# Kernel tuning notes

Hardware: AMD Instinct MI355X
Metric: run time of the kernel (lower is better)

## Reference

```python
import jax, jax.numpy as jnp
import numpy as np

SEQ_LEN = 2048

def setup_inputs() -> dict:
    key = jax.random.key(0)
    kq, kk, kv = jax.random.split(key, 3)
    B, S, D = 8, SEQ_LEN, 64
    q = jax.random.normal(kq, (B, S, D), dtype=jnp.float32)
    k = jax.random.normal(kk, (B, S, D), dtype=jnp.float32)
    v = jax.random.normal(kv, (B, S, D), dtype=jnp.float32)
    return {"q": q, "k": k, "v": v}

def reference(q, k, v):
    # scores: [B, S, S] = q @ k^T  (note: original applies NO 1/sqrt(d) scaling)
    scores = jnp.einsum('bqd,bkd->bqk', q, k)
    S = scores.shape[-1]
    causal = jnp.tril(jnp.ones((S, S), dtype=bool))  # lower-triangular mask
    scores = jnp.where(causal, scores, -jnp.inf)
    weights = jax.nn.softmax(scores, axis=-1)
    return jnp.einsum('bqk,bkd->bqd', weights, v)
```

## Files before the change

kernel.cpp:

```cpp
#include <hip/hip_runtime.h>


#define BATCH 8
#define SEQ 2048
#define DIM 64
#define NEL (BATCH * SEQ * DIM)

typedef __attribute__((ext_vector_type(8))) short short8;
typedef __attribute__((ext_vector_type(4))) float f32x4;

#define MFMA(a, b, c) __builtin_amdgcn_mfma_f32_16x16x32_bf16(a, b, c, 0, 0, 0)

__device__ __forceinline__ unsigned short f2bf(float x) {
    unsigned u = __float_as_uint(x);
    unsigned r = u + 0x7fffu + ((u >> 16) & 1u);
    return (unsigned short)(r >> 16);
}
__device__ __forceinline__ float bf2f(unsigned short h) {
    return __uint_as_float(((unsigned)h) << 16);
}
__device__ __forceinline__ short8 ld8(const unsigned short* p) {
    return *(const short8*)p;
}

__device__ __forceinline__ float dpp_max16(float x) {
    float o;
    o = __int_as_float(__builtin_amdgcn_update_dpp(0, __float_as_int(x), 0xB1, 0xF, 0xF, true));
    x = fmaxf(x, o);
    o = __int_as_float(__builtin_amdgcn_update_dpp(0, __float_as_int(x), 0x4E, 0xF, 0xF, true));
    x = fmaxf(x, o);
    o = __int_as_float(__builtin_amdgcn_update_dpp(0, __float_as_int(x), 0x141, 0xF, 0xF, true));
    x = fmaxf(x, o);
    o = __int_as_float(__builtin_amdgcn_update_dpp(0, __float_as_int(x), 0x140, 0xF, 0xF, true));
    return fmaxf(x, o);
}
__device__ __forceinline__ float dpp_sum16(float x) {
    float o;
    o = __int_as_float(__builtin_amdgcn_update_dpp(0, __float_as_int(x), 0xB1, 0xF, 0xF, true));
    x += o;
    o = __int_as_float(__builtin_amdgcn_update_dpp(0, __float_as_int(x), 0x4E, 0xF, 0xF, true));
    x += o;
    o = __int_as_float(__builtin_amdgcn_update_dpp(0, __float_as_int(x), 0x141, 0xF, 0xF, true));
    x += o;
    o = __int_as_float(__builtin_amdgcn_update_dpp(0, __float_as_int(x), 0x140, 0xF, 0xF, true));
    return x + o;
}

__global__ __launch_bounds__(256) void prep(
    const float* __restrict__ Q, const float* __restrict__ K,
    const float* __restrict__ V,
    unsigned short* __restrict__ Qh, unsigned short* __restrict__ Ql,
    unsigned short* __restrict__ Kh, unsigned short* __restrict__ Kl,
    unsigned short* __restrict__ Vf)
{
    __shared__ unsigned short sT[64][72];
    const int blk = blockIdx.x;
    const int t = threadIdx.x;

    if (blk < 2048) {
        const int idx = (blk * 256 + t) * 4;
        const float* src; unsigned short *dh, *dl; int off;
        if (idx < NEL) { src = Q; dh = Qh; dl = Ql; off = idx; }
        else           { src = K; dh = Kh; dl = Kl; off = idx - NEL; }
        float4 v = *(const float4*)(src + off);
        ushort4 h, l;
        h.x = f2bf(v.x); l.x = f2bf(v.x - bf2f(h.x));
        h.y = f2bf(v.y); l.y = f2bf(v.y - bf2f(h.y));
        h.z = f2bf(v.z); l.z = f2bf(v.z - bf2f(h.z));
        h.w = f2bf(v.w); l.w = f2bf(v.w - bf2f(h.w));
        *(ushort4*)(dh + off) = h;
        *(ushort4*)(dl + off) = l;
        return;
    }

    const int tile = blk - 2048;
    const int b = tile >> 5;
    const int s0 = (tile & 31) * 64;
    const int srow = t >> 4;
    const int d4   = (t & 15) * 4;
#pragma unroll
    for (int i = 0; i < 4; ++i) {
        const int row = srow + i * 16;
        float4 v = *(const float4*)(V + ((size_t)(b * SEQ + s0 + row)) * DIM + d4);
        sT[d4 + 0][row] = f2bf(v.x);
        sT[d4 + 1][row] = f2bf(v.y);
        sT[d4 + 2][row] = f2bf(v.z);
        sT[d4 + 3][row] = f2bf(v.w);
    }
    __syncthreads();
#pragma unroll
    for (int i = 0; i < 2; ++i) {
        const int fid = t + i * 256;
        const int cc  = fid >> 8;
        const int nt  = (fid >> 6) & 3;
        const int l   = fid & 63;
        const int key = cc * 32 + (l >> 4) * 8;
        const int dim = nt * 16 + (l & 15);
        const int c   = (s0 >> 5) + cc;
        unsigned short* dst =
            Vf + ((((size_t)(b * 64 + c)) * 4 + nt) << 9) + l * 8;
        *(float4*)dst = *(const float4*)&sT[dim][key];
    }
}

__global__ __launch_bounds__(256) void attn_main(
    const unsigned short* __restrict__ Qh, const unsigned short* __restrict__ Ql,
    const unsigned short* __restrict__ Kh, const unsigned short* __restrict__ Kl,
    const unsigned short* __restrict__ Vf, float* __restrict__ O)
{
    __shared__ __align__(16) char scratch[4][4352];
    __shared__ float sMl[4][16][2];

    const int bid  = blockIdx.x;
    const int b    = bid & (BATCH - 1);
    const int pair = bid >> 3;

    const int t    = threadIdx.x;
    const int w    = t >> 6;
    const int lane = t & 63;
    const int quad = lane >> 4;
    const int n16  = lane & 15;
    const int boff = b * SEQ;

    unsigned short* sPw = (unsigned short*)scratch[w];
    float*          sOw = (float*)scratch[w];

    for (int half = 0; half < 2; ++half) {
        const int qt = half ? (127 - pair) : pair;
        const int q0 = qt * 16;
        const int q_max = q0 + 15;

        const unsigned short* qp  = Qh + ((size_t)(boff + q0 + n16)) * DIM + quad * 8;
        const unsigned short* qlp = Ql + ((size_t)(boff + q0 + n16)) * DIM + quad * 8;
        short8 qh0 = ld8(qp),  qh1 = ld8(qp + 32);
        short8 ql0 = ld8(qlp), ql1 = ld8(qlp + 32);

        float m0 = -1e30f, m1 = -1e30f, m2 = -1e30f, m3 = -1e30f;
        float l0 = 0.f, l1 = 0.f, l2 = 0.f, l3 = 0.f;
        f32x4 oacc[4];
#pragma unroll
        for (int i = 0; i < 4; ++i) oacc[i] = (f32x4){0.f, 0.f, 0.f, 0.f};

        for (int kb = w * 128; kb <= q_max; kb += 512) {
            const int rem  = q_max - kb;
            const int nsub = min(8, (rem >> 4) + 1);
            const int nchain = (nsub + 1) >> 1;
            f32x4 sacc[8];

#pragma unroll
            for (int gp = 0; gp < 4; ++gp) {
                const int stA = 2 * gp, stB = stA + 1;
                if (stA < nsub) {
                    const size_t krA = (size_t)(boff + kb + stA * 16 + n16) * DIM + quad * 8;
                    short8 khA0 = ld8(Kh + krA), khA1 = ld8(Kh + krA + 32);
                    short8 klA0 = ld8(Kl + krA), klA1 = ld8(Kl + krA + 32);
                    const bool okB = (stB < nsub);
                    const size_t krB = (size_t)(boff + kb + stB * 16 + n16) * DIM + quad * 8;
                    short8 khB0, khB1, klB0, klB1;
                    if (okB) {
                        khB0 = ld8(Kh + krB); khB1 = ld8(Kh + krB + 32);
                        klB0 = ld8(Kl + krB); klB1 = ld8(Kl + krB + 32);
                    }
                    f32x4 accA = (f32x4){0.f, 0.f, 0.f, 0.f};
                    accA = MFMA(qh0, khA0, accA);
                    accA = MFMA(qh1, khA1, accA);
                    accA = MFMA(qh0, klA0, accA);
                    accA = MFMA(qh1, klA1, accA);
                    accA = MFMA(ql0, khA0, accA);
                    accA = MFMA(ql1, khA1, accA);
                    sacc[stA] = accA;
                    if (okB) {
                        f32x4 accB = (f32x4){0.f, 0.f, 0.f, 0.f};
                        accB = MFMA(qh0, khB0, accB);
                        accB = MFMA(qh1, khB1, accB);
                        accB = MFMA(qh0, klB0, accB);
                        accB = MFMA(qh1, klB1, accB);
                        accB = MFMA(ql0, khB0, accB);
                        accB = MFMA(ql1, khB1, accB);
                        sacc[stB] = accB;
                    } else {
                        sacc[stB] = (f32x4){-1e30f, -1e30f, -1e30f, -1e30f};
                    }
                } else {
                    sacc[stA] = (f32x4){-1e30f, -1e30f, -1e30f, -1e30f};
                    sacc[stB] = (f32x4){-1e30f, -1e30f, -1e30f, -1e30f};
                }
            }

            if (kb + 127 > q0) {
#pragma unroll
                for (int st = 0; st < 8; ++st) {
                    if (st < nsub) {
                        const int key = kb + st * 16 + n16;
#pragma unroll
                        for (int r = 0; r < 4; ++r)
                            if (key > q0 + quad * 4 + r) sacc[st][r] = -1e30f;
                    }
                }
            }

            float mt0 = sacc[0][0], mt1 = sacc[0][1], mt2 = sacc[0][2], mt3 = sacc[0][3];
#pragma unroll
            for (int st = 1; st < 8; ++st) {
                mt0 = fmaxf(mt0, sacc[st][0]);
                mt1 = fmaxf(mt1, sacc[st][1]);
                mt2 = fmaxf(mt2, sacc[st][2]);
                mt3 = fmaxf(mt3, sacc[st][3]);
            }
            mt0 = dpp_max16(mt0); mt1 = dpp_max16(mt1);
            mt2 = dpp_max16(mt2); mt3 = dpp_max16(mt3);
            const float mn0 = fmaxf(m0, mt0), mn1 = fmaxf(m1, mt1);
            const float mn2 = fmaxf(m2, mt2), mn3 = fmaxf(m3, mt3);
            const float a0 = __expf(m0 - mn0), a1 = __expf(m1 - mn1);
            const float a2 = __expf(m2 - mn2), a3 = __expf(m3 - mn3);
            m0 = mn0; m1 = mn1; m2 = mn2; m3 = mn3;

            float ps0 = 0.f, ps1 = 0.f, ps2 = 0.f, ps3 = 0.f;
            const int stmax = 2 * nchain;
#pragma unroll
            for (int st = 0; st < 8; ++st) {
                if (st < stmax) {
                    float p0 = 0.f, p1 = 0.f, p2 = 0.f, p3 = 0.f;
                    if (st < nsub) {
                        p0 = __expf(sacc[st][0] - mn0);
                        p1 = __expf(sacc[st][1] - mn1);
                        p2 = __expf(sacc[st][2] - mn2);
                        p3 = __expf(sacc[st][3] - mn3);
                        ps0 += p0; ps1 += p1; ps2 += p2; ps3 += p3;
                    }
                    const int col = st * 16 + n16;
                    sPw[(quad * 4 + 0) * 136 + col] = f2bf(p0);
                    sPw[(quad * 4 + 1) * 136 + col] = f2bf(p1);
                    sPw[(quad * 4 + 2) * 136 + col] = f2bf(p2);
                    sPw[(quad * 4 + 3) * 136 + col] = f2bf(p3);
                }
            }
            ps0 = dpp_sum16(ps0); ps1 = dpp_sum16(ps1);
            ps2 = dpp_sum16(ps2); ps3 = dpp_sum16(ps3);
            l0 = l0 * a0 + ps0; l1 = l1 * a1 + ps1;
            l2 = l2 * a2 + ps2; l3 = l3 * a3 + ps3;
#pragma unroll
            for (int nt = 0; nt < 4; ++nt) {
                oacc[nt][0] *= a0; oacc[nt][1] *= a1;
                oacc[nt][2] *= a2; oacc[nt][3] *= a3;
            }

#pragma unroll
            for (int ch = 0; ch < 4; ++ch) {
                if (ch < nchain) {
                    short8 pa = ld8(&sPw[n16 * 136 + ch * 32 + quad * 8]);
                    const size_t cbase =
                        (((size_t)(b * 64 + (kb >> 5) + ch)) * 4) << 9;
#pragma unroll
                    for (int nt = 0; nt < 4; ++nt) {
                        short8 vv = ld8(Vf + cbase + (nt << 9) + lane * 8);
                        oacc[nt] = MFMA(pa, vv, oacc[nt]);
                    }
                }
            }
        }

#pragma unroll
        for (int nt = 0; nt < 4; ++nt)
#pragma unroll
            for (int r = 0; r < 4; ++r)
                sOw[(quad * 4 + r) * 68 + nt * 16 + n16] = oacc[nt][r];
        if (n16 == 0) {
            sMl[w][quad * 4 + 0][0] = m0; sMl[w][quad * 4 + 0][1] = l0;
            sMl[w][quad * 4 + 1][0] = m1; sMl[w][quad * 4 + 1][1] = l1;
            sMl[w][quad * 4 + 2][0] = m2; sMl[w][quad * 4 + 2][1] = l2;
            sMl[w][quad * 4 + 3][0] = m3; sMl[w][quad * 4 + 3][1] = l3;
        }
        __syncthreads();

        const int row  = t >> 4;
        const int col4 = (t & 15) * 4;
        float M = fmaxf(fmaxf(sMl[0][row][0], sMl[1][row][0]),
                        fmaxf(sMl[2][row][0], sMl[3][row][0]));
        float L = 0.f;
        float ox = 0.f, oy = 0.f, oz = 0.f, ow = 0.f;
#pragma unroll
        for (int wv = 0; wv < 4; ++wv) {
            const float ew = __expf(sMl[wv][row][0] - M);
            L += ew * sMl[wv][row][1];
            const float* op = (const float*)scratch[wv] + row * 68 + col4;
            ox += ew * op[0]; oy += ew * op[1]; oz += ew * op[2]; ow += ew * op[3];
        }
        const float inv = 1.0f / L;
        float4 res = make_float4(ox * inv, oy * inv, oz * inv, ow * inv);
        *(float4*)(O + ((size_t)(boff + q0 + row)) * DIM + col4) = res;

        __syncthreads();
    }
}

extern "C" void kernel_launch(void* const* d_in, const int* in_sizes, int n_in,
                              void* d_out, int out_size, void* d_ws, size_t ws_size,
                              hipStream_t stream) {
    const float* q = (const float*)d_in[0];
    const float* k = (const float*)d_in[1];
    const float* v = (const float*)d_in[2];
    float* out = (float*)d_out;

    unsigned short* Qh = (unsigned short*)d_ws;
    unsigned short* Ql = Qh + NEL;
    unsigned short* Kh = Ql + NEL;
    unsigned short* Kl = Kh + NEL;
    unsigned short* Vf = Kl + NEL;

    prep<<<dim3(2048 + 256), dim3(256), 0, stream>>>(q, k, v, Qh, Ql, Kh, Kl, Vf);
    attn_main<<<dim3(512), dim3(256), 0, stream>>>(Qh, Ql, Kh, Kl, Vf, out);
}
```

Measured before the change: 112.5 us.

## Process paired low and high query tiles jointly to share K/V loads

Instead of looping over the two paired query tiles one after another, each block now keeps both tiles' accumulators live and walks the key range once. K and V fragments loaded for the long (high) tile are reused for the short (low) tile, which roughly halves global K/V traffic for the overlapping part. The block-to-pair mapping is also permuted so consecutive blocks get interleaved pair indices. In exchange register pressure roughly doubles (two sets of Q fragments, score tiles and output accumulators), and an extra LDS buffer is added, which may reduce occupancy or cause spills.

```diff
diff --git a/kernel.cpp b/kernel.cpp
--- a/kernel.cpp
+++ b/kernel.cpp
@@ -109,11 +109,15 @@
     const unsigned short* __restrict__ Vf, float* __restrict__ O)
 {
     __shared__ __align__(16) char scratch[4][4352];
+    __shared__ __align__(16) unsigned short sPL[4][16][136];
     __shared__ float sMl[4][16][2];
 
-    const int bid  = blockIdx.x;
-    const int b    = bid & (BATCH - 1);
-    const int pair = bid >> 3;
+    const int bid = blockIdx.x;
+    const int b   = bid & (BATCH - 1);
+    const int jj  = bid >> 3;
+    const int j   = (jj < 32) ? jj : 95 - jj;
+    const int q0L = j * 16,        q_maxL = q0L + 15;
+    const int q0H = (127 - j) * 16, q_maxH = q0H + 15;
 
     const int t    = threadIdx.x;
     const int w    = t >> 6;
@@ -124,109 +128,155 @@
 
     unsigned short* sPw = (unsigned short*)scratch[w];
     float*          sOw = (float*)scratch[w];
-
-    for (int half = 0; half < 2; ++half) {
-        const int qt = half ? (127 - pair) : pair;
-        const int q0 = qt * 16;
-        const int q_max = q0 + 15;
-
-        const unsigned short* qp  = Qh + ((size_t)(boff + q0 + n16)) * DIM + quad * 8;
-        const unsigned short* qlp = Ql + ((size_t)(boff + q0 + n16)) * DIM + quad * 8;
-        short8 qh0 = ld8(qp),  qh1 = ld8(qp + 32);
-        short8 ql0 = ld8(qlp), ql1 = ld8(qlp + 32);
-
-        float m0 = -1e30f, m1 = -1e30f, m2 = -1e30f, m3 = -1e30f;
-        float l0 = 0.f, l1 = 0.f, l2 = 0.f, l3 = 0.f;
-        f32x4 oacc[4];
-#pragma unroll
-        for (int i = 0; i < 4; ++i) oacc[i] = (f32x4){0.f, 0.f, 0.f, 0.f};
-
-        for (int kb = w * 128; kb <= q_max; kb += 512) {
-            const int rem  = q_max - kb;
-            const int nsub = min(8, (rem >> 4) + 1);
-            const int nchain = (nsub + 1) >> 1;
-            f32x4 sacc[8];
-
-#pragma unroll
-            for (int gp = 0; gp < 4; ++gp) {
-                const int stA = 2 * gp, stB = stA + 1;
-                if (stA < nsub) {
-                    const size_t krA = (size_t)(boff + kb + stA * 16 + n16) * DIM + quad * 8;
-                    short8 khA0 = ld8(Kh + krA), khA1 = ld8(Kh + krA + 32);
-                    short8 klA0 = ld8(Kl + krA), klA1 = ld8(Kl + krA + 32);
-                    const bool okB = (stB < nsub);
-                    const size_t krB = (size_t)(boff + kb + stB * 16 + n16) * DIM + quad * 8;
-                    short8 khB0, khB1, klB0, klB1;
-                    if (okB) {
-                        khB0 = ld8(Kh + krB); khB1 = ld8(Kh + krB + 32);
-                        klB0 = ld8(Kl + krB); klB1 = ld8(Kl + krB + 32);
-                    }
-                    f32x4 accA = (f32x4){0.f, 0.f, 0.f, 0.f};
-                    accA = MFMA(qh0, khA0, accA);
-                    accA = MFMA(qh1, khA1, accA);
-                    accA = MFMA(qh0, klA0, accA);
-                    accA = MFMA(qh1, klA1, accA);
-                    accA = MFMA(ql0, khA0, accA);
-                    accA = MFMA(ql1, khA1, accA);
-                    sacc[stA] = accA;
-                    if (okB) {
-                        f32x4 accB = (f32x4){0.f, 0.f, 0.f, 0.f};
-                        accB = MFMA(qh0, khB0, accB);
-                        accB = MFMA(qh1, khB1, accB);
-                        accB = MFMA(qh0, klB0, accB);
-                        accB = MFMA(qh1, klB1, accB);
-                        accB = MFMA(ql0, khB0, accB);
-                        accB = MFMA(ql1, khB1, accB);
-                        sacc[stB] = accB;
+    unsigned short* sPLw = &sPL[w][0][0];
+
+    const unsigned short* qpL  = Qh + ((size_t)(boff + q0L + n16)) * DIM + quad * 8;
+    const unsigned short* qlpL = Ql + ((size_t)(boff + q0L + n16)) * DIM + quad * 8;
+    short8 qh0L = ld8(qpL),  qh1L = ld8(qpL + 32);
+    short8 ql0L = ld8(qlpL), ql1L = ld8(qlpL + 32);
+    const unsigned short* qpH  = Qh + ((size_t)(boff + q0H + n16)) * DIM + quad * 8;
+    const unsigned short* qlpH = Ql + ((size_t)(boff + q0H + n16)) * DIM + quad * 8;
+    short8 qh0H = ld8(qpH),  qh1H = ld8(qpH + 32);
+    short8 ql0H = ld8(qlpH), ql1H = ld8(qlpH + 32);
+
+    float mL0 = -1e30f, mL1 = -1e30f, mL2 = -1e30f, mL3 = -1e30f;
+    float lL0 = 0.f, lL1 = 0.f, lL2 = 0.f, lL3 = 0.f;
+    float mH0 = -1e30f, mH1 = -1e30f, mH2 = -1e30f, mH3 = -1e30f;
+    float lH0 = 0.f, lH1 = 0.f, lH2 = 0.f, lH3 = 0.f;
+    f32x4 oL[4], oH[4];
+#pragma unroll
+    for (int i = 0; i < 4; ++i) {
+        oL[i] = (f32x4){0.f, 0.f, 0.f, 0.f};
+        oH[i] = (f32x4){0.f, 0.f, 0.f, 0.f};
+    }
+
+    for (int kb = w * 128; kb <= q_maxH; kb += 512) {
+        const int nsubH   = min(8, ((q_maxH - kb) >> 4) + 1);
+        const int nchainH = (nsubH + 1) >> 1;
+        const bool lact   = (kb <= q_maxL);
+        const int nsubL   = lact ? min(8, ((q_maxL - kb) >> 4) + 1) : 0;
+        const int nchainL = (nsubL + 1) >> 1;
+
+        f32x4 sH[8], sL[8];
+
+#pragma unroll
+        for (int gp = 0; gp < 4; ++gp) {
+            const int stA = 2 * gp, stB = stA + 1;
+            if (stA < nsubH) {
+                const size_t krA = (size_t)(boff + kb + stA * 16 + n16) * DIM + quad * 8;
+                short8 khA0 = ld8(Kh + krA), khA1 = ld8(Kh + krA + 32);
+                short8 klA0 = ld8(Kl + krA), klA1 = ld8(Kl + krA + 32);
+                const bool okB = (stB < nsubH);
+                const size_t krB = (size_t)(boff + kb + stB * 16 + n16) * DIM + quad * 8;
+                short8 khB0, khB1, klB0, klB1;
+                if (okB) {
+                    khB0 = ld8(Kh + krB); khB1 = ld8(Kh + krB + 32);
+                    klB0 = ld8(Kl + krB); klB1 = ld8(Kl + krB + 32);
+                }
+                {
+                    f32x4 acc = (f32x4){0.f, 0.f, 0.f, 0.f};
+                    acc = MFMA(qh0H, khA0, acc);
+                    acc = MFMA(qh1H, khA1, acc);
+                    acc = MFMA(qh0H, klA0, acc);
+                    acc = MFMA(qh1H, klA1, acc);
+                    acc = MFMA(ql0H, khA0, acc);
+                    acc = MFMA(ql1H, khA1, acc);
+                    sH[stA] = acc;
+                }
+                if (stA < nsubL) {
+                    f32x4 acc = (f32x4){0.f, 0.f, 0.f, 0.f};
+                    acc = MFMA(qh0L, khA0, acc);
+                    acc = MFMA(qh1L, khA1, acc);
+                    acc = MFMA(qh0L, klA0, acc);
+                    acc = MFMA(qh1L, klA1, acc);
+                    acc = MFMA(ql0L, khA0, acc);
+                    acc = MFMA(ql1L, khA1, acc);
+                    sL[stA] = acc;
+                } else {
+                    sL[stA] = (f32x4){-1e30f, -1e30f, -1e30f, -1e30f};
+                }
+                if (okB) {
+                    f32x4 acc = (f32x4){0.f, 0.f, 0.f, 0.f};
+                    acc = MFMA(qh0H, khB0, acc);
+                    acc = MFMA(qh1H, khB1, acc);
+                    acc = MFMA(qh0H, klB0, acc);
+                    acc = MFMA(qh1H, klB1, acc);
+                    acc = MFMA(ql0H, khB0, acc);
+                    acc = MFMA(ql1H, khB1, acc);
+                    sH[stB] = acc;
+                    if (stB < nsubL) {
+                        f32x4 acc2 = (f32x4){0.f, 0.f, 0.f, 0.f};
+                        acc2 = MFMA(qh0L, khB0, acc2);
+                        acc2 = MFMA(qh1L, khB1, acc2);
+                        acc2 = MFMA(qh0L, klB0, acc2);
+                        acc2 = MFMA(qh1L, klB1, acc2);
+                        acc2 = MFMA(ql0L, khB0, acc2);
+                        acc2 = MFMA(ql1L, khB1, acc2);
+                        sL[stB] = acc2;
                     } else {
-                        sacc[stB] = (f32x4){-1e30f, -1e30f, -1e30f, -1e30f};
+                        sL[stB] = (f32x4){-1e30f, -1e30f, -1e30f, -1e30f};
                     }
                 } else {
-                    sacc[stA] = (f32x4){-1e30f, -1e30f, -1e30f, -1e30f};
-                    sacc[stB] = (f32x4){-1e30f, -1e30f, -1e30f, -1e30f};
-                }
-            }
-
-            if (kb + 127 > q0) {
-#pragma unroll
-                for (int st = 0; st < 8; ++st) {
-                    if (st < nsub) {
-                        const int key = kb + st * 16 + n16;
-#pragma unroll
-                        for (int r = 0; r < 4; ++r)
-                            if (key > q0 + quad * 4 + r) sacc[st][r] = -1e30f;
-                    }
-                }
-            }
-
-            float mt0 = sacc[0][0], mt1 = sacc[0][1], mt2 = sacc[0][2], mt3 = sacc[0][3];
+                    sH[stB] = (f32x4){-1e30f, -1e30f, -1e30f, -1e30f};
+                    sL[stB] = (f32x4){-1e30f, -1e30f, -1e30f, -1e30f};
+                }
+            } else {
+                sH[stA] = (f32x4){-1e30f, -1e30f, -1e30f, -1e30f};
+                sH[stB] = (f32x4){-1e30f, -1e30f, -1e30f, -1e30f};
+                sL[stA] = (f32x4){-1e30f, -1e30f, -1e30f, -1e30f};
+                sL[stB] = (f32x4){-1e30f, -1e30f, -1e30f, -1e30f};
+            }
+        }
+
+        if (kb + 127 > q0H) {
+#pragma unroll
+            for (int st = 0; st < 8; ++st) {
+                if (st < nsubH) {
+                    const int key = kb + st * 16 + n16;
+#pragma unroll
+                    for (int r = 0; r < 4; ++r)
+                        if (key > q0H + quad * 4 + r) sH[st][r] = -1e30f;
+                }
+            }
+        }
+        if (lact && (kb + 127 > q0L)) {
+#pragma unroll
+            for (int st = 0; st < 8; ++st) {
+                if (st < nsubL) {
+                    const int key = kb + st * 16 + n16;
+#pragma unroll
+                    for (int r = 0; r < 4; ++r)
+                        if (key > q0L + quad * 4 + r) sL[st][r] = -1e30f;
+                }
+            }
+        }
+
+        {
+            float t0 = sH[0][0], t1 = sH[0][1], t2 = sH[0][2], t3 = sH[0][3];
 #pragma unroll
             for (int st = 1; st < 8; ++st) {
-                mt0 = fmaxf(mt0, sacc[st][0]);
-                mt1 = fmaxf(mt1, sacc[st][1]);
-                mt2 = fmaxf(mt2, sacc[st][2]);
-                mt3 = fmaxf(mt3, sacc[st][3]);
-            }
-            mt0 = dpp_max16(mt0); mt1 = dpp_max16(mt1);
-            mt2 = dpp_max16(mt2); mt3 = dpp_max16(mt3);
-            const float mn0 = fmaxf(m0, mt0), mn1 = fmaxf(m1, mt1);
-            const float mn2 = fmaxf(m2, mt2), mn3 = fmaxf(m3, mt3);
-            const float a0 = __expf(m0 - mn0), a1 = __expf(m1 - mn1);
-            const float a2 = __expf(m2 - mn2), a3 = __expf(m3 - mn3);
-            m0 = mn0; m1 = mn1; m2 = mn2; m3 = mn3;
-
-            float ps0 = 0.f, ps1 = 0.f, ps2 = 0.f, ps3 = 0.f;
-            const int stmax = 2 * nchain;
+                t0 = fmaxf(t0, sH[st][0]); t1 = fmaxf(t1, sH[st][1]);
+                t2 = fmaxf(t2, sH[st][2]); t3 = fmaxf(t3, sH[st][3]);
+            }
+            t0 = dpp_max16(t0); t1 = dpp_max16(t1);
+            t2 = dpp_max16(t2); t3 = dpp_max16(t3);
+            const float n0 = fmaxf(mH0, t0), n1 = fmaxf(mH1, t1);
+            const float n2 = fmaxf(mH2, t2), n3 = fmaxf(mH3, t3);
+            const float a0 = __expf(mH0 - n0), a1 = __expf(mH1 - n1);
+            const float a2 = __expf(mH2 - n2), a3 = __expf(mH3 - n3);
+            mH0 = n0; mH1 = n1; mH2 = n2; mH3 = n3;
+            float p0s = 0.f, p1s = 0.f, p2s = 0.f, p3s = 0.f;
+            const int stmax = 2 * nchainH;
 #pragma unroll
             for (int st = 0; st < 8; ++st) {
                 if (st < stmax) {
                     float p0 = 0.f, p1 = 0.f, p2 = 0.f, p3 = 0.f;
-                    if (st < nsub) {
-                        p0 = __expf(sacc[st][0] - mn0);
-                        p1 = __expf(sacc[st][1] - mn1);
-                        p2 = __expf(sacc[st][2] - mn2);
-                        p3 = __expf(sacc[st][3] - mn3);
-                        ps0 += p0; ps1 += p1; ps2 += p2; ps3 += p3;
+                    if (st < nsubH) {
+                        p0 = __expf(sH[st][0] - n0);
+                        p1 = __expf(sH[st][1] - n1);
+                        p2 = __expf(sH[st][2] - n2);
+                        p3 = __expf(sH[st][3] - n3);
+                        p0s += p0; p1s += p1; p2s += p2; p3s += p3;
                     }
                     const int col = st * 16 + n16;
                     sPw[(quad * 4 + 0) * 136 + col] = f2bf(p0);
@@ -235,61 +285,128 @@
                     sPw[(quad * 4 + 3) * 136 + col] = f2bf(p3);
                 }
             }
-            ps0 = dpp_sum16(ps0); ps1 = dpp_sum16(ps1);
-            ps2 = dpp_sum16(ps2); ps3 = dpp_sum16(ps3);
-            l0 = l0 * a0 + ps0; l1 = l1 * a1 + ps1;
-            l2 = l2 * a2 + ps2; l3 = l3 * a3 + ps3;
+            p0s = dpp_sum16(p0s); p1s = dpp_sum16(p1s);
+            p2s = dpp_sum16(p2s); p3s = dpp_sum16(p3s);
+            lH0 = lH0 * a0 + p0s; lH1 = lH1 * a1 + p1s;
+            lH2 = lH2 * a2 + p2s; lH3 = lH3 * a3 + p3s;
 #pragma unroll
             for (int nt = 0; nt < 4; ++nt) {
-                oacc[nt][0] *= a0; oacc[nt][1] *= a1;
-                oacc[nt][2] *= a2; oacc[nt][3] *= a3;
-            }
-
-#pragma unroll
-            for (int ch = 0; ch < 4; ++ch) {
-                if (ch < nchain) {
-                    short8 pa = ld8(&sPw[n16 * 136 + ch * 32 + quad * 8]);
-                    const size_t cbase =
-                        (((size_t)(b * 64 + (kb >> 5) + ch)) * 4) << 9;
-#pragma unroll
-                    for (int nt = 0; nt < 4; ++nt) {
-                        short8 vv = ld8(Vf + cbase + (nt << 9) + lane * 8);
-                        oacc[nt] = MFMA(pa, vv, oacc[nt]);
+                oH[nt][0] *= a0; oH[nt][1] *= a1;
+                oH[nt][2] *= a2; oH[nt][3] *= a3;
+            }
+        }
+
+        if (lact) {
+            float t0 = sL[0][0], t1 = sL[0][1], t2 = sL[0][2], t3 = sL[0][3];
+#pragma unroll
+            for (int st = 1; st < 8; ++st) {
+                t0 = fmaxf(t0, sL[st][0]); t1 = fmaxf(t1, sL[st][1]);
+                t2 = fmaxf(t2, sL[st][2]); t3 = fmaxf(t3, sL[st][3]);
+            }
+            t0 = dpp_max16(t0); t1 = dpp_max16(t1);
+            t2 = dpp_max16(t2); t3 = dpp_max16(t3);
+            const float n0 = fmaxf(mL0, t0), n1 = fmaxf(mL1, t1);
+            const float n2 = fmaxf(mL2, t2), n3 = fmaxf(mL3, t3);
+            const float a0 = __expf(mL0 - n0), a1 = __expf(mL1 - n1);
+            const float a2 = __expf(mL2 - n2), a3 = __expf(mL3 - n3);
+            mL0 = n0; mL1 = n1; mL2 = n2; mL3 = n3;
+            float p0s = 0.f, p1s = 0.f, p2s = 0.f, p3s = 0.f;
+            const int stmax = 2 * nchainL;
+#pragma unroll
+            for (int st = 0; st < 8; ++st) {
+                if (st < stmax) {
+                    float p0 = 0.f, p1 = 0.f, p2 = 0.f, p3 = 0.f;
+                    if (st < nsubL) {
+                        p0 = __expf(sL[st][0] - n0);
+                        p1 = __expf(sL[st][1] - n1);
+                        p2 = __expf(sL[st][2] - n2);
+                        p3 = __expf(sL[st][3] - n3);
+                        p0s += p0; p1s += p1; p2s += p2; p3s += p3;
                     }
-                }
-            }
-        }
-
+                    const int col = st * 16 + n16;
+                    sPLw[(quad * 4 + 0) * 136 + col] = f2bf(p0);
+                    sPLw[(quad * 4 + 1) * 136 + col] = f2bf(p1);
+                    sPLw[(quad * 4 + 2) * 136 + col] = f2bf(p2);
+                    sPLw[(quad * 4 + 3) * 136 + col] = f2bf(p3);
+                }
+            }
+            p0s = dpp_sum16(p0s); p1s = dpp_sum16(p1s);
+            p2s = dpp_sum16(p2s); p3s = dpp_sum16(p3s);
+            lL0 = lL0 * a0 + p0s; lL1 = lL1 * a1 + p1s;
+            lL2 = lL2 * a2 + p2s; lL3 = lL3 * a3 + p3s;
+#pragma unroll
+            for (int nt = 0; nt < 4; ++nt) {
+                oL[nt][0] *= a0; oL[nt][1] *= a1;
+                oL[nt][2] *= a2; oL[nt][3] *= a3;
+            }
+        }
+
+#pragma unroll
+        for (int ch = 0; ch < 4; ++ch) {
+            if (ch < nchainH) {
+                const size_t cbase =
+                    (((size_t)(b * 64 + (kb >> 5) + ch)) * 4) << 9;
+                short8 v0 = ld8(Vf + cbase + (0 << 9) + lane * 8);
+                short8 v1 = ld8(Vf + cbase + (1 << 9) + lane * 8);
+                short8 v2 = ld8(Vf + cbase + (2 << 9) + lane * 8);
+                short8 v3 = ld8(Vf + cbase + (3 << 9) + lane * 8);
+                if (ch < nchainL) {
+                    short8 pl = ld8(&sPLw[n16 * 136 + ch * 32 + quad * 8]);
+                    oL[0] = MFMA(pl, v0, oL[0]);
+                    oL[1] = MFMA(pl, v1, oL[1]);
+                    oL[2] = MFMA(pl, v2, oL[2]);
+                    oL[3] = MFMA(pl, v3, oL[3]);
+                }
+                short8 ph = ld8(&sPw[n16 * 136 + ch * 32 + quad * 8]);
+                oH[0] = MFMA(ph, v0, oH[0]);
+                oH[1] = MFMA(ph, v1, oH[1]);
+                oH[2] = MFMA(ph, v2, oH[2]);
+                oH[3] = MFMA(ph, v3, oH[3]);
+            }
+        }
+    }
+
+    const int row  = t >> 4;
+    const int col4 = (t & 15) * 4;
+#pragma unroll
+    for (int tile = 0; tile < 2; ++tile) {
+        const f32x4* oo = tile ? oH : oL;
 #pragma unroll
         for (int nt = 0; nt < 4; ++nt)
 #pragma unroll
             for (int r = 0; r < 4; ++r)
-                sOw[(quad * 4 + r) * 68 + nt * 16 + n16] = oacc[nt][r];
+                sOw[(quad * 4 + r) * 68 + nt * 16 + n16] = oo[nt][r];
         if (n16 == 0) {
-            sMl[w][quad * 4 + 0][0] = m0; sMl[w][quad * 4 + 0][1] = l0;
-            sMl[w][quad * 4 + 1][0] = m1; sMl[w][quad * 4 + 1][1] = l1;
-            sMl[w][quad * 4 + 2][0] = m2; sMl[w][quad * 4 + 2][1] = l2;
-            sMl[w][quad * 4 + 3][0] = m3; sMl[w][quad * 4 + 3][1] = l3;
+            if (tile) {
+                sMl[w][quad * 4 + 0][0] = mH0; sMl[w][quad * 4 + 0][1] = lH0;
+                sMl[w][quad * 4 + 1][0] = mH1; sMl[w][quad * 4 + 1][1] = lH1;
+                sMl[w][quad * 4 + 2][0] = mH2; sMl[w][quad * 4 + 2][1] = lH2;
+                sMl[w][quad * 4 + 3][0] = mH3; sMl[w][quad * 4 + 3][1] = lH3;
+            } else {
+                sMl[w][quad * 4 + 0][0] = mL0; sMl[w][quad * 4 + 0][1] = lL0;
+                sMl[w][quad * 4 + 1][0] = mL1; sMl[w][quad * 4 + 1][1] = lL1;
+                sMl[w][quad * 4 + 2][0] = mL2; sMl[w][quad * 4 + 2][1] = lL2;
+                sMl[w][quad * 4 + 3][0] = mL3; sMl[w][quad * 4 + 3][1] = lL3;
+            }
         }
         __syncthreads();
-
-        const int row  = t >> 4;
-        const int col4 = (t & 15) * 4;
-        float M = fmaxf(fmaxf(sMl[0][row][0], sMl[1][row][0]),
-                        fmaxf(sMl[2][row][0], sMl[3][row][0]));
-        float L = 0.f;
-        float ox = 0.f, oy = 0.f, oz = 0.f, ow = 0.f;
-#pragma unroll
-        for (int wv = 0; wv < 4; ++wv) {
-            const float ew = __expf(sMl[wv][row][0] - M);
-            L += ew * sMl[wv][row][1];
-            const float* op = (const float*)scratch[wv] + row * 68 + col4;
-            ox += ew * op[0]; oy += ew * op[1]; oz += ew * op[2]; ow += ew * op[3];
-        }
-        const float inv = 1.0f / L;
-        float4 res = make_float4(ox * inv, oy * inv, oz * inv, ow * inv);
-        *(float4*)(O + ((size_t)(boff + q0 + row)) * DIM + col4) = res;
-
+        {
+            float M = fmaxf(fmaxf(sMl[0][row][0], sMl[1][row][0]),
+                            fmaxf(sMl[2][row][0], sMl[3][row][0]));
+            float L = 0.f;
+            float ox = 0.f, oy = 0.f, oz = 0.f, ow = 0.f;
+#pragma unroll
+            for (int wv = 0; wv < 4; ++wv) {
+                const float ew = __expf(sMl[wv][row][0] - M);
+                L += ew * sMl[wv][row][1];
+                const float* op = (const float*)scratch[wv] + row * 68 + col4;
+                ox += ew * op[0]; oy += ew * op[1]; oz += ew * op[2]; ow += ew * op[3];
+            }
+            const float inv = 1.0f / L;
+            const int q0 = tile ? q0H : q0L;
+            float4 res = make_float4(ox * inv, oy * inv, oz * inv, ow * inv);
+            *(float4*)(O + ((size_t)(boff + q0 + row)) * DIM + col4) = res;
+        }
         __syncthreads();
     }
 }
```

Result: slower. 115.9 us (+3.1%).
